# Kernel tuning notes

Measured on AMD Instinct MI355X. Metric: run time of the kernel, lower is better.

Reference implementation:

```python
import jax, jax.numpy as jnp
import numpy as np

NEG_SLOPE = 0.1


def _conv3d(x, w, b):
    # standard 3x3x3 conv, stride 1, pad 1, NCDHW layout
    y = jax.lax.conv_general_dilated(
        x, w, window_strides=(1, 1, 1), padding=[(1, 1), (1, 1), (1, 1)],
        dimension_numbers=('NCDHW', 'OIDHW', 'NCDHW'))
    return y + b[None, :, None, None, None]


def _deform_conv3d_hw(x, w_off, b_off, w, b):
    """DeformConvPack_d with dimension='HW': 3x3x3 conv whose H/W sampling
    positions are shifted by learned per-location offsets (bilinear sample in
    H,W; integer taps in D). Zero padding outside the volume."""
    B, C, D, H, W = x.shape
    # offset conv: 2 offsets (dh, dw) per kernel tap, 27 taps -> 54 channels
    off = _conv3d(x, w_off, b_off).reshape(B, 27, 2, D, H, W)
    x_flat = x.reshape(B, C, D * H * W)
    d_grid = jnp.arange(D)[:, None, None]          # [D,1,1]
    h_grid = jnp.arange(H)[None, :, None]          # [1,H,1]
    w_grid = jnp.arange(W)[None, None, :]          # [1,1,W]
    out = jnp.zeros((B, w.shape[0], D, H, W), x.dtype)
    k = 0
    for kd in (-1, 0, 1):
        pd = d_grid + kd                            # integer depth tap
        valid_d = (pd >= 0) & (pd < D)
        pdc = jnp.clip(pd, 0, D - 1)
        for kh in (-1, 0, 1):
            for kw in (-1, 0, 1):
                ph = h_grid + kh + off[:, k, 0]     # [B,D,H,W] float
                pw = w_grid + kw + off[:, k, 1]
                h0 = jnp.floor(ph)
                w0 = jnp.floor(pw)
                th = ph - h0                        # bilinear fracs
                tw = pw - w0
                h0i = h0.astype(jnp.int32)
                w0i = w0.astype(jnp.int32)
                samp = jnp.zeros((B, C, D, H, W), x.dtype)
                for dh, wgt_h in ((0, 1.0 - th), (1, th)):
                    hh = h0i + dh
                    vh = (hh >= 0) & (hh < H)
                    hhc = jnp.clip(hh, 0, H - 1)
                    for dw, wgt_w in ((0, 1.0 - tw), (1, tw)):
                        ww = w0i + dw
                        v = valid_d & vh & (ww >= 0) & (ww < W)
                        wwc = jnp.clip(ww, 0, W - 1)
                        idx = (pdc * H + hhc) * W + wwc          # [B,D,H,W]
                        g = jnp.take_along_axis(
                            x_flat, idx.reshape(B, 1, D * H * W), axis=2
                        ).reshape(B, C, D, H, W)
                        wgt = jnp.where(v, wgt_h * wgt_w, 0.0)
                        samp = samp + g * wgt[:, None]
                # accumulate this tap's contribution through the conv weight
                out = out + jnp.einsum('bcdhw,oc->bodhw', samp,
                                       w[:, :, kd + 1, kh + 1, kw + 1])
                k += 1
    return out + b[None, :, None, None, None]


def setup_inputs() -> dict:
    key = jax.random.key(0)
    ks = jax.random.split(key, 9)
    B, nf, D, H, W = 4, 48, 12, 56, 56
    fan = 1.0 / np.sqrt(nf * 27)
    x = jax.random.normal(ks[0], (B, nf, D, H, W), jnp.float32)
    # offset convs: small weights so sampled offsets stay O(1) pixel
    w_off0 = jax.random.normal(ks[1], (54, nf, 3, 3, 3), jnp.float32) * 0.01
    b_off0 = jax.random.normal(ks[2], (54,), jnp.float32) * 0.01
    w0 = jax.random.normal(ks[3], (nf, nf, 3, 3, 3), jnp.float32) * fan
    b0 = jax.random.normal(ks[4], (nf,), jnp.float32) * 0.01
    w_off1 = jax.random.normal(ks[5], (54, nf, 3, 3, 3), jnp.float32) * 0.01
    b_off1 = jax.random.normal(ks[6], (54,), jnp.float32) * 0.01
    w1 = jax.random.normal(ks[7], (nf, nf, 3, 3, 3), jnp.float32) * fan
    b1 = jax.random.normal(ks[8], (nf,), jnp.float32) * 0.01
    return {"x": x, "w_off0": w_off0, "b_off0": b_off0, "w0": w0, "b0": b0,
            "w_off1": w_off1, "b_off1": b_off1, "w1": w1, "b1": b1}


def reference(x, w_off0, b_off0, w0, b0, w_off1, b_off1, w1, b1):
    h = _deform_conv3d_hw(x, w_off0, b_off0, w0, b0)
    h = jnp.where(h >= 0, h, NEG_SLOPE * h)  # LeakyReLU(0.1)
    y = _deform_conv3d_hw(h, w_off1, b_off1, w1, b1)
    return y + x
```

## Files before the change

### kernel.cpp

```cpp
#include <hip/hip_runtime.h>
#include <hip/hip_bf16.h>

constexpr int B_ = 4, C_ = 48, D_ = 12, H_ = 56, W_ = 56;
constexpr int DHW_ = D_ * H_ * W_;
constexpr int NLOC_ = B_ * DHW_;
constexpr int OFFC_ = 54;
constexpr int NXCD_ = 8;

typedef short bf16x8 __attribute__((ext_vector_type(8)));
typedef float f32x4  __attribute__((ext_vector_type(4)));
typedef unsigned int u32x4 __attribute__((ext_vector_type(4)));
typedef unsigned int u32x2 __attribute__((ext_vector_type(2)));

__device__ __forceinline__ int xcd_swizzle(int bid, int nwg) {
    int xcd = bid % NXCD_, lid = bid / NXCD_;
    int q = nwg / NXCD_, r = nwg % NXCD_;
    return (xcd < r ? xcd * (q + 1) : r * (q + 1) + (xcd - r) * q) + lid;
}

__device__ __forceinline__ unsigned int f2bf_u(float f) {
    __hip_bfloat16 h = __float2bfloat16(f);
    return (unsigned int)__builtin_bit_cast(unsigned short, h);
}
__device__ __forceinline__ float bflo(unsigned int pv) {
    return __builtin_bit_cast(float, pv << 16);
}
__device__ __forceinline__ float bfhi(unsigned int pv) {
    return __builtin_bit_cast(float, pv & 0xffff0000u);
}

__device__ __forceinline__ u32x4 interp4(u32x4 c00, u32x4 c01, u32x4 c10, u32x4 c11,
                                         f32x4 cw) {
    u32x4 pv;
#pragma unroll
    for (int u = 0; u < 4; ++u) {
        float lo = cw[0] * bflo(c00[u]);
        lo = fmaf(cw[1], bflo(c01[u]), lo);
        lo = fmaf(cw[2], bflo(c10[u]), lo);
        lo = fmaf(cw[3], bflo(c11[u]), lo);
        float hi = cw[0] * bfhi(c00[u]);
        hi = fmaf(cw[1], bfhi(c01[u]), hi);
        hi = fmaf(cw[2], bfhi(c10[u]), hi);
        hi = fmaf(cw[3], bfhi(c11[u]), hi);
        pv[u] = f2bf_u(lo) | (f2bf_u(hi) << 16);
    }
    return pv;
}

__global__ void __launch_bounds__(256) repack_frag_kernel(
    const float* __restrict__ w, unsigned short* __restrict__ wf, int OC, int MT) {
    int t = blockIdx.x * 256 + threadIdx.x;
    int total = 27 * MT * 1024;
    if (t >= total) return;
    int i    = t & 7;
    int lane = (t >> 3) & 63;
    int ks   = (t >> 9) & 1;
    int mt   = (t >> 10) % MT;
    int k    = t / (MT << 10);
    int oc = mt * 16 + (lane & 15);
    int c  = ks * 32 + 8 * (lane >> 4) + i;
    float v = (oc < OC && c < 48) ? w[((size_t)oc * 48 + c) * 27 + k] : 0.0f;
    wf[t] = (unsigned short)f2bf_u(v);
}

__global__ void __launch_bounds__(256) to_cl_kernel(const float* __restrict__ x,
                                                    unsigned short* __restrict__ xcl) {
    int loc = blockIdx.x * 256 + threadIdx.x;
    int b = loc / DHW_, s = loc - b * DHW_;
    const float* xp = x + (size_t)b * (C_ * DHW_) + s;
#pragma unroll
    for (int q = 0; q < 6; ++q) {
        float v[8];
#pragma unroll
        for (int u = 0; u < 8; ++u) v[u] = xp[(size_t)(q * 8 + u) * DHW_];
        u32x4 o;
#pragma unroll
        for (int u = 0; u < 4; ++u)
            o[u] = f2bf_u(v[2 * u]) | (f2bf_u(v[2 * u + 1]) << 16);
        *(u32x4*)(xcl + ((size_t)q * NLOC_ + loc) * 8) = o;
    }
}

__global__ void __launch_bounds__(128) offconv_mfma(
    const unsigned short* __restrict__ xcl,
    const unsigned short* __restrict__ wf,
    const float* __restrict__ bo,
    float* __restrict__ off) {
    __shared__ unsigned short S[2][64][64];
    int tid = threadIdx.x, wid = tid >> 6, lane = tid & 63;
    int base = xcd_swizzle(blockIdx.x, gridDim.x) * 64;
    int loc = base + lane;
    int b = loc / DHW_;
    int sp = loc - b * DHW_;
    int w = sp % W_; int t1 = sp / W_;
    int h = t1 % H_; int d = t1 / H_;
    int g = lane >> 4, li = lane & 15, l7 = lane & 7;

    u32x4 z = {0, 0, 0, 0};
    *(u32x4*)&S[wid][lane][(6 ^ l7) * 8] = z;
    *(u32x4*)&S[wid][lane][(7 ^ l7) * 8] = z;

    f32x4 acc[4][4];
#pragma unroll
    for (int mt = 0; mt < 4; ++mt)
#pragma unroll
        for (int nt = 0; nt < 4; ++nt) acc[mt][nt] = (f32x4){0.f, 0.f, 0.f, 0.f};

    const u32x4* plane[6];
#pragma unroll
    for (int q = 0; q < 6; ++q)
        plane[q] = (const u32x4*)(xcl + ((size_t)q * NLOC_ + (size_t)b * DHW_) * 8);

#pragma unroll 1
    for (int i = 0; i < 14; ++i) {
        int k = wid + 2 * i;
        if (k >= 27) break;
        int kd = k / 9 - 1, kh = (k / 3) % 3 - 1, kw = k % 3 - 1;
        int pd = d + kd, ph = h + kh, pw = w + kw;
        bool valid = (pd >= 0) & (pd < D_) & (ph >= 0) & (ph < H_) & (pw >= 0) & (pw < W_);
        int pdc = min(max(pd, 0), D_ - 1);
        int phc = min(max(ph, 0), H_ - 1);
        int pwc = min(max(pw, 0), W_ - 1);
        int pix = (pdc * H_ + phc) * W_ + pwc;
        u32x4 pv[6];
#pragma unroll
        for (int cc = 0; cc < 6; ++cc) pv[cc] = plane[cc][pix];
#pragma unroll
        for (int cc = 0; cc < 6; ++cc) {
            if (!valid) pv[cc] = z;
            *(u32x4*)&S[wid][lane][(cc ^ l7) * 8] = pv[cc];
        }
        const unsigned short* wk = wf + (size_t)k * 4096 + lane * 8;
        bf16x8 a[4][2];
#pragma unroll
        for (int mt = 0; mt < 4; ++mt)
#pragma unroll
            for (int ks = 0; ks < 2; ++ks)
                a[mt][ks] = *(const bf16x8*)&wk[(mt * 2 + ks) * 512];
#pragma unroll
        for (int nt = 0; nt < 4; ++nt) {
            const unsigned short* sr = &S[wid][nt * 16 + li][0];
            bf16x8 b0 = *(const bf16x8*)&sr[((0 + g) ^ l7) * 8];
            bf16x8 b1 = *(const bf16x8*)&sr[((4 + g) ^ l7) * 8];
#pragma unroll
            for (int mt = 0; mt < 4; ++mt) {
                acc[mt][nt] = __builtin_amdgcn_mfma_f32_16x16x32_bf16(a[mt][0], b0, acc[mt][nt], 0, 0, 0);
                acc[mt][nt] = __builtin_amdgcn_mfma_f32_16x16x32_bf16(a[mt][1], b1, acc[mt][nt], 0, 0, 0);
            }
        }
    }

    float* XCH = (float*)&S[0][0][0];
    __syncthreads();
    if (wid == 1) {
#pragma unroll
        for (int mt = 0; mt < 2; ++mt)
#pragma unroll
            for (int nt = 0; nt < 4; ++nt)
                *(f32x4*)(XCH + (mt * 4 + nt) * 256 + lane * 4) = acc[mt][nt];
    }
    __syncthreads();
    if (wid == 0) {
#pragma unroll
        for (int mt = 0; mt < 2; ++mt)
#pragma unroll
            for (int nt = 0; nt < 4; ++nt)
                acc[mt][nt] += *(f32x4*)(XCH + (mt * 4 + nt) * 256 + lane * 4);
    }
    __syncthreads();
    if (wid == 1) {
#pragma unroll
        for (int mt = 2; mt < 4; ++mt)
#pragma unroll
            for (int nt = 0; nt < 4; ++nt)
                *(f32x4*)(XCH + ((mt - 2) * 4 + nt) * 256 + lane * 4) = acc[mt][nt];
    }
    __syncthreads();
    if (wid == 1) return;
#pragma unroll
    for (int mt = 2; mt < 4; ++mt)
#pragma unroll
        for (int nt = 0; nt < 4; ++nt)
            acc[mt][nt] += *(f32x4*)(XCH + ((mt - 2) * 4 + nt) * 256 + lane * 4);

    int s0 = base - b * DHW_;
#pragma unroll
    for (int mt = 0; mt < 4; ++mt) {
#pragma unroll
        for (int r = 0; r < 4; ++r) {
            int oc = mt * 16 + 4 * g + r;
            if (oc < OFFC_) {
                float bb = bo[oc];
#pragma unroll
                for (int nt = 0; nt < 4; ++nt) {
                    size_t addr = ((size_t)b * OFFC_ + oc) * DHW_ + (s0 + nt * 16 + li);
                    off[addr] = acc[mt][nt][r] + bb;
                }
            }
        }
    }
}

template <int LEAKY, int RESID, int CLOUT>
__global__ void __launch_bounds__(128) deform_mfma(
    const unsigned short* __restrict__ scl,
    const float* __restrict__ off,
    const unsigned short* __restrict__ wf,
    const float* __restrict__ bias,
    const float* __restrict__ resid,
    float* __restrict__ dstf,
    unsigned short* __restrict__ dstcl) {
    __shared__ unsigned short S[2][64][64];
    int tid = threadIdx.x, wid = tid >> 6, lane = tid & 63;
    int base = xcd_swizzle(blockIdx.x, gridDim.x) * 64;
    int loc = base + lane;
    int b = loc / DHW_;
    int sp = loc - b * DHW_;
    int w = sp % W_; int t1 = sp / W_;
    int h = t1 % H_; int d = t1 / H_;
    int g = lane >> 4, li = lane & 15, l7 = lane & 7;

    u32x4 z = {0, 0, 0, 0};
    *(u32x4*)&S[wid][lane][(6 ^ l7) * 8] = z;
    *(u32x4*)&S[wid][lane][(7 ^ l7) * 8] = z;

    f32x4 acc[3][4];
#pragma unroll
    for (int mt = 0; mt < 3; ++mt)
#pragma unroll
        for (int nt = 0; nt < 4; ++nt) acc[mt][nt] = (f32x4){0.f, 0.f, 0.f, 0.f};

    const u32x4* plane[6];
#pragma unroll
    for (int q = 0; q < 6; ++q)
        plane[q] = (const u32x4*)(scl + ((size_t)q * NLOC_ + (size_t)b * DHW_) * 8);
    const float* ob = off + (size_t)b * (OFFC_ * DHW_) + sp;

#pragma unroll 1
    for (int i = 0; i < 14; ++i) {
        int k = wid + 2 * i;
        if (k >= 27) break;
        int kd = k / 9 - 1, kh = (k / 3) % 3 - 1, kw = k % 3 - 1;
        int pd = d + kd;
        bool vd = (pd >= 0) & (pd < D_);
        int pdc = min(max(pd, 0), D_ - 1);

        float odh = ob[(size_t)(2 * k + 0) * DHW_];
        float odw = ob[(size_t)(2 * k + 1) * DHW_];
        float phf = (float)(h + kh) + odh;
        float pwf = (float)(w + kw) + odw;
        float h0f = floorf(phf), w0f = floorf(pwf);
        float th = phf - h0f, tw = pwf - w0f;
        int h0 = (int)h0f, w0 = (int)w0f;

        int pix[4];
        f32x4 cw;
#pragma unroll
        for (int dh = 0; dh < 2; ++dh) {
            int hh = h0 + dh;
            bool vh = vd & (hh >= 0) & (hh < H_);
            int hhc = min(max(hh, 0), H_ - 1);
            float wh = dh ? th : 1.0f - th;
#pragma unroll
            for (int dw = 0; dw < 2; ++dw) {
                int ww = w0 + dw;
                bool v = vh & (ww >= 0) & (ww < W_);
                int wwc = min(max(ww, 0), W_ - 1);
                float wwt = dw ? tw : 1.0f - tw;
                pix[dh * 2 + dw] = (pdc * H_ + hhc) * W_ + wwc;
                cw[dh * 2 + dw] = v ? wh * wwt : 0.0f;
            }
        }

#pragma unroll
        for (int half = 0; half < 2; ++half) {
            u32x4 st[3][4];
#pragma unroll
            for (int cc = 0; cc < 3; ++cc)
#pragma unroll
                for (int j = 0; j < 4; ++j)
                    st[cc][j] = plane[half * 3 + cc][pix[j]];
#pragma unroll
            for (int cc = 0; cc < 3; ++cc) {
                u32x4 pv = interp4(st[cc][0], st[cc][1], st[cc][2], st[cc][3], cw);
                *(u32x4*)&S[wid][lane][((half * 3 + cc) ^ l7) * 8] = pv;
            }
        }

        const unsigned short* wk = wf + (size_t)k * 3072 + lane * 8;
        bf16x8 a[3][2];
#pragma unroll
        for (int mt = 0; mt < 3; ++mt)
#pragma unroll
            for (int ks = 0; ks < 2; ++ks)
                a[mt][ks] = *(const bf16x8*)&wk[(mt * 2 + ks) * 512];
#pragma unroll
        for (int nt = 0; nt < 4; ++nt) {
            const unsigned short* sr = &S[wid][nt * 16 + li][0];
            bf16x8 b0 = *(const bf16x8*)&sr[((0 + g) ^ l7) * 8];
            bf16x8 b1 = *(const bf16x8*)&sr[((4 + g) ^ l7) * 8];
#pragma unroll
            for (int mt = 0; mt < 3; ++mt) {
                acc[mt][nt] = __builtin_amdgcn_mfma_f32_16x16x32_bf16(a[mt][0], b0, acc[mt][nt], 0, 0, 0);
                acc[mt][nt] = __builtin_amdgcn_mfma_f32_16x16x32_bf16(a[mt][1], b1, acc[mt][nt], 0, 0, 0);
            }
        }
    }

    float* XCH = (float*)&S[1][0][0];
    __syncthreads();
    if (wid == 1) {
#pragma unroll
        for (int mt = 0; mt < 2; ++mt)
#pragma unroll
            for (int nt = 0; nt < 4; ++nt)
                *(f32x4*)(XCH + (mt * 4 + nt) * 256 + lane * 4) = acc[mt][nt];
    }
    __syncthreads();
    if (wid == 0) {
#pragma unroll
        for (int mt = 0; mt < 2; ++mt)
#pragma unroll
            for (int nt = 0; nt < 4; ++nt)
                acc[mt][nt] += *(f32x4*)(XCH + (mt * 4 + nt) * 256 + lane * 4);
    }
    __syncthreads();
    if (wid == 1) {
#pragma unroll
        for (int nt = 0; nt < 4; ++nt)
            *(f32x4*)(XCH + nt * 256 + lane * 4) = acc[2][nt];
    }
    __syncthreads();
    if (wid == 1) return;
#pragma unroll
    for (int nt = 0; nt < 4; ++nt)
        acc[2][nt] += *(f32x4*)(XCH + nt * 256 + lane * 4);

    if (CLOUT) {
        unsigned short* Sb = &S[0][0][0];
#pragma unroll
        for (int mt = 0; mt < 3; ++mt) {
#pragma unroll
            for (int nt = 0; nt < 4; ++nt) {
                float v[4];
#pragma unroll
                for (int r = 0; r < 4; ++r) {
                    int oc = mt * 16 + 4 * g + r;
                    float t = acc[mt][nt][r] + bias[oc];
                    if (LEAKY) t = (t >= 0.f) ? t : 0.1f * t;
                    v[r] = t;
                }
                int row = nt * 16 + li;
                int colb = (mt * 32 + 8 * g) ^ ((li & 7) << 4);
                u32x2 pp = {f2bf_u(v[0]) | (f2bf_u(v[1]) << 16),
                            f2bf_u(v[2]) | (f2bf_u(v[3]) << 16)};
                *(u32x2*)((char*)(Sb + (size_t)row * 64) + colb) = pp;
            }
        }
        unsigned short* myrow = Sb + (size_t)lane * 64;
#pragma unroll
        for (int s = 0; s < 6; ++s) {
            u32x4 c = *(u32x4*)((char*)myrow + ((s * 16) ^ ((lane & 7) << 4)));
            *(u32x4*)(dstcl + ((size_t)s * NLOC_ + loc) * 8) = c;
        }
    } else {
        int s0 = base - b * DHW_;
#pragma unroll
        for (int mt = 0; mt < 3; ++mt) {
#pragma unroll
            for (int r = 0; r < 4; ++r) {
                int oc = mt * 16 + 4 * g + r;
                float bb = bias[oc];
#pragma unroll
                for (int nt = 0; nt < 4; ++nt) {
                    size_t addr = ((size_t)b * C_ + oc) * DHW_ + (s0 + nt * 16 + li);
                    float v = acc[mt][nt][r] + bb;
                    if (LEAKY) v = (v >= 0.0f) ? v : 0.1f * v;
                    if (RESID) v += resid[addr];
                    dstf[addr] = v;
                }
            }
        }
    }
}

extern "C" void kernel_launch(void* const* d_in, const int* in_sizes, int n_in,
                              void* d_out, int out_size, void* d_ws, size_t ws_size,
                              hipStream_t stream) {
    const float* x      = (const float*)d_in[0];
    const float* w_off0 = (const float*)d_in[1];
    const float* b_off0 = (const float*)d_in[2];
    const float* w0     = (const float*)d_in[3];
    const float* b0     = (const float*)d_in[4];
    const float* w_off1 = (const float*)d_in[5];
    const float* b_off1 = (const float*)d_in[6];
    const float* w1     = (const float*)d_in[7];
    const float* b1     = (const float*)d_in[8];
    float* out = (float*)d_out;

    float* off_buf = (float*)d_ws;
    unsigned short* xcl = (unsigned short*)(off_buf + (size_t)OFFC_ * NLOC_);
    unsigned short* hcl = xcl + (size_t)NLOC_ * 48;
    unsigned short* wf_off  = hcl + (size_t)NLOC_ * 48;
    unsigned short* wf_conv = wf_off + 27 * 4 * 1024;

    dim3 blk128(128), blk256(256);
    int nblk = NLOC_ / 64;

    to_cl_kernel<<<NLOC_ / 256, blk256, 0, stream>>>(x, xcl);

    repack_frag_kernel<<<(27 * 4 * 1024 + 255) / 256, blk256, 0, stream>>>(w_off0, wf_off, OFFC_, 4);
    repack_frag_kernel<<<(27 * 3 * 1024 + 255) / 256, blk256, 0, stream>>>(w0, wf_conv, C_, 3);
    offconv_mfma<<<nblk, blk128, 0, stream>>>(xcl, wf_off, b_off0, off_buf);
    deform_mfma<1, 0, 1><<<nblk, blk128, 0, stream>>>(xcl, off_buf, wf_conv, b0, nullptr, nullptr, hcl);

    repack_frag_kernel<<<(27 * 4 * 1024 + 255) / 256, blk256, 0, stream>>>(w_off1, wf_off, OFFC_, 4);
    repack_frag_kernel<<<(27 * 3 * 1024 + 255) / 256, blk256, 0, stream>>>(w1, wf_conv, C_, 3);
    offconv_mfma<<<nblk, blk128, 0, stream>>>(hcl, wf_off, b_off1, off_buf);
    deform_mfma<0, 1, 0><<<nblk, blk128, 0, stream>>>(hcl, off_buf, wf_conv, b1, x, out, nullptr);
}
```

Before: 296.8 us.

## Fuse offset conv into deformable conv kernel via shared-memory offset tile

Merges the offset-convolution kernel and the deformable-convolution kernel into one per-layer kernel. Offsets for each 64-location tile are computed with MFMA, biased, and stored in a shared-memory tile, so the deform stage reads them from LDS instead of a global offset buffer. This removes the global write and read of the 54-channel fp32 offset tensor and one launch per layer. It also skips kernel taps that are invalid for the whole wavefront. The cost is extra LDS use (about 15 KB more per block), which may lower occupancy, plus more registers and syncs in a single kernel.

```diff
diff --git a/kernel.cpp b/kernel.cpp
--- a/kernel.cpp
+++ b/kernel.cpp
@@ -9,6 +9,7 @@
 
 typedef short bf16x8 __attribute__((ext_vector_type(8)));
 typedef float f32x4  __attribute__((ext_vector_type(4)));
+typedef float f32x2  __attribute__((ext_vector_type(2)));
 typedef unsigned int u32x4 __attribute__((ext_vector_type(4)));
 typedef unsigned int u32x2 __attribute__((ext_vector_type(2)));
 
@@ -81,12 +82,18 @@
     }
 }
 
-__global__ void __launch_bounds__(128) offconv_mfma(
-    const unsigned short* __restrict__ xcl,
-    const unsigned short* __restrict__ wf,
+template <int LEAKY, int RESID, int CLOUT>
+__global__ void __launch_bounds__(128) fused_layer(
+    const unsigned short* __restrict__ scl,
+    const unsigned short* __restrict__ wfo,
     const float* __restrict__ bo,
-    float* __restrict__ off) {
+    const unsigned short* __restrict__ wfc,
+    const float* __restrict__ bias,
+    const float* __restrict__ resid,
+    float* __restrict__ dstf,
+    unsigned short* __restrict__ dstcl) {
     __shared__ unsigned short S[2][64][64];
+    __shared__ __align__(16) float OFT[64][58];
     int tid = threadIdx.x, wid = tid >> 6, lane = tid & 63;
     int base = xcd_swizzle(blockIdx.x, gridDim.x) * 64;
     int loc = base + lane;
@@ -100,127 +107,108 @@
     *(u32x4*)&S[wid][lane][(6 ^ l7) * 8] = z;
     *(u32x4*)&S[wid][lane][(7 ^ l7) * 8] = z;
 
-    f32x4 acc[4][4];
-#pragma unroll
-    for (int mt = 0; mt < 4; ++mt)
-#pragma unroll
-        for (int nt = 0; nt < 4; ++nt) acc[mt][nt] = (f32x4){0.f, 0.f, 0.f, 0.f};
-
     const u32x4* plane[6];
 #pragma unroll
     for (int q = 0; q < 6; ++q)
-        plane[q] = (const u32x4*)(xcl + ((size_t)q * NLOC_ + (size_t)b * DHW_) * 8);
+        plane[q] = (const u32x4*)(scl + ((size_t)q * NLOC_ + (size_t)b * DHW_) * 8);
+
+    {
+        f32x4 acc[4][4];
+#pragma unroll
+        for (int mt = 0; mt < 4; ++mt)
+#pragma unroll
+            for (int nt = 0; nt < 4; ++nt) acc[mt][nt] = (f32x4){0.f, 0.f, 0.f, 0.f};
 
 #pragma unroll 1
-    for (int i = 0; i < 14; ++i) {
-        int k = wid + 2 * i;
-        if (k >= 27) break;
-        int kd = k / 9 - 1, kh = (k / 3) % 3 - 1, kw = k % 3 - 1;
-        int pd = d + kd, ph = h + kh, pw = w + kw;
-        bool valid = (pd >= 0) & (pd < D_) & (ph >= 0) & (ph < H_) & (pw >= 0) & (pw < W_);
-        int pdc = min(max(pd, 0), D_ - 1);
-        int phc = min(max(ph, 0), H_ - 1);
-        int pwc = min(max(pw, 0), W_ - 1);
-        int pix = (pdc * H_ + phc) * W_ + pwc;
-        u32x4 pv[6];
-#pragma unroll
-        for (int cc = 0; cc < 6; ++cc) pv[cc] = plane[cc][pix];
-#pragma unroll
-        for (int cc = 0; cc < 6; ++cc) {
-            if (!valid) pv[cc] = z;
-            *(u32x4*)&S[wid][lane][(cc ^ l7) * 8] = pv[cc];
-        }
-        const unsigned short* wk = wf + (size_t)k * 4096 + lane * 8;
-        bf16x8 a[4][2];
-#pragma unroll
-        for (int mt = 0; mt < 4; ++mt)
-#pragma unroll
-            for (int ks = 0; ks < 2; ++ks)
-                a[mt][ks] = *(const bf16x8*)&wk[(mt * 2 + ks) * 512];
-#pragma unroll
-        for (int nt = 0; nt < 4; ++nt) {
-            const unsigned short* sr = &S[wid][nt * 16 + li][0];
-            bf16x8 b0 = *(const bf16x8*)&sr[((0 + g) ^ l7) * 8];
-            bf16x8 b1 = *(const bf16x8*)&sr[((4 + g) ^ l7) * 8];
-#pragma unroll
-            for (int mt = 0; mt < 4; ++mt) {
-                acc[mt][nt] = __builtin_amdgcn_mfma_f32_16x16x32_bf16(a[mt][0], b0, acc[mt][nt], 0, 0, 0);
-                acc[mt][nt] = __builtin_amdgcn_mfma_f32_16x16x32_bf16(a[mt][1], b1, acc[mt][nt], 0, 0, 0);
-            }
-        }
-    }
-
-    float* XCH = (float*)&S[0][0][0];
-    __syncthreads();
-    if (wid == 1) {
-#pragma unroll
-        for (int mt = 0; mt < 2; ++mt)
-#pragma unroll
-            for (int nt = 0; nt < 4; ++nt)
-                *(f32x4*)(XCH + (mt * 4 + nt) * 256 + lane * 4) = acc[mt][nt];
-    }
-    __syncthreads();
-    if (wid == 0) {
-#pragma unroll
-        for (int mt = 0; mt < 2; ++mt)
-#pragma unroll
-            for (int nt = 0; nt < 4; ++nt)
-                acc[mt][nt] += *(f32x4*)(XCH + (mt * 4 + nt) * 256 + lane * 4);
-    }
-    __syncthreads();
-    if (wid == 1) {
-#pragma unroll
-        for (int mt = 2; mt < 4; ++mt)
-#pragma unroll
-            for (int nt = 0; nt < 4; ++nt)
-                *(f32x4*)(XCH + ((mt - 2) * 4 + nt) * 256 + lane * 4) = acc[mt][nt];
-    }
-    __syncthreads();
-    if (wid == 1) return;
-#pragma unroll
-    for (int mt = 2; mt < 4; ++mt)
-#pragma unroll
-        for (int nt = 0; nt < 4; ++nt)
-            acc[mt][nt] += *(f32x4*)(XCH + ((mt - 2) * 4 + nt) * 256 + lane * 4);
-
-    int s0 = base - b * DHW_;
-#pragma unroll
-    for (int mt = 0; mt < 4; ++mt) {
-#pragma unroll
-        for (int r = 0; r < 4; ++r) {
-            int oc = mt * 16 + 4 * g + r;
-            if (oc < OFFC_) {
-                float bb = bo[oc];
-#pragma unroll
-                for (int nt = 0; nt < 4; ++nt) {
-                    size_t addr = ((size_t)b * OFFC_ + oc) * DHW_ + (s0 + nt * 16 + li);
-                    off[addr] = acc[mt][nt][r] + bb;
+        for (int i = 0; i < 14; ++i) {
+            int k = wid + 2 * i;
+            if (k >= 27) break;
+            int kd = k / 9 - 1, kh = (k / 3) % 3 - 1, kw = k % 3 - 1;
+            int pd = d + kd, ph = h + kh, pw = w + kw;
+            bool valid = (pd >= 0) & (pd < D_) & (ph >= 0) & (ph < H_) &
+                         (pw >= 0) & (pw < W_);
+            if (!__any((int)valid)) continue;
+            int pdc = min(max(pd, 0), D_ - 1);
+            int phc = min(max(ph, 0), H_ - 1);
+            int pwc = min(max(pw, 0), W_ - 1);
+            int pix = (pdc * H_ + phc) * W_ + pwc;
+            u32x4 pv[6];
+#pragma unroll
+            for (int cc = 0; cc < 6; ++cc) pv[cc] = plane[cc][pix];
+#pragma unroll
+            for (int cc = 0; cc < 6; ++cc) {
+                if (!valid) pv[cc] = z;
+                *(u32x4*)&S[wid][lane][(cc ^ l7) * 8] = pv[cc];
+            }
+            const unsigned short* wk = wfo + (size_t)k * 4096 + lane * 8;
+            bf16x8 a[4][2];
+#pragma unroll
+            for (int mt = 0; mt < 4; ++mt)
+#pragma unroll
+                for (int ks = 0; ks < 2; ++ks)
+                    a[mt][ks] = *(const bf16x8*)&wk[(mt * 2 + ks) * 512];
+#pragma unroll
+            for (int nt = 0; nt < 4; ++nt) {
+                const unsigned short* sr = &S[wid][nt * 16 + li][0];
+                bf16x8 b0 = *(const bf16x8*)&sr[((0 + g) ^ l7) * 8];
+                bf16x8 b1 = *(const bf16x8*)&sr[((4 + g) ^ l7) * 8];
+#pragma unroll
+                for (int mt = 0; mt < 4; ++mt) {
+                    acc[mt][nt] = __builtin_amdgcn_mfma_f32_16x16x32_bf16(a[mt][0], b0, acc[mt][nt], 0, 0, 0);
+                    acc[mt][nt] = __builtin_amdgcn_mfma_f32_16x16x32_bf16(a[mt][1], b1, acc[mt][nt], 0, 0, 0);
                 }
             }
         }
-    }
-}
-
-template <int LEAKY, int RESID, int CLOUT>
-__global__ void __launch_bounds__(128) deform_mfma(
-    const unsigned short* __restrict__ scl,
-    const float* __restrict__ off,
-    const unsigned short* __restrict__ wf,
-    const float* __restrict__ bias,
-    const float* __restrict__ resid,
-    float* __restrict__ dstf,
-    unsigned short* __restrict__ dstcl) {
-    __shared__ unsigned short S[2][64][64];
-    int tid = threadIdx.x, wid = tid >> 6, lane = tid & 63;
-    int base = xcd_swizzle(blockIdx.x, gridDim.x) * 64;
-    int loc = base + lane;
-    int b = loc / DHW_;
-    int sp = loc - b * DHW_;
-    int w = sp % W_; int t1 = sp / W_;
-    int h = t1 % H_; int d = t1 / H_;
-    int g = lane >> 4, li = lane & 15, l7 = lane & 7;
-
-    u32x4 z = {0, 0, 0, 0};
+
+        float* XCH = (float*)&S[0][0][0];
+        __syncthreads();
+        if (wid == 1) {
+#pragma unroll
+            for (int mt = 0; mt < 2; ++mt)
+#pragma unroll
+                for (int nt = 0; nt < 4; ++nt)
+                    *(f32x4*)(XCH + (mt * 4 + nt) * 256 + lane * 4) = acc[mt][nt];
+        }
+        __syncthreads();
+        if (wid == 0) {
+#pragma unroll
+            for (int mt = 0; mt < 2; ++mt)
+#pragma unroll
+                for (int nt = 0; nt < 4; ++nt)
+                    acc[mt][nt] += *(f32x4*)(XCH + (mt * 4 + nt) * 256 + lane * 4);
+        }
+        __syncthreads();
+        if (wid == 1) {
+#pragma unroll
+            for (int mt = 2; mt < 4; ++mt)
+#pragma unroll
+                for (int nt = 0; nt < 4; ++nt)
+                    *(f32x4*)(XCH + ((mt - 2) * 4 + nt) * 256 + lane * 4) = acc[mt][nt];
+        }
+        __syncthreads();
+        if (wid == 0) {
+#pragma unroll
+            for (int mt = 2; mt < 4; ++mt)
+#pragma unroll
+                for (int nt = 0; nt < 4; ++nt)
+                    acc[mt][nt] += *(f32x4*)(XCH + ((mt - 2) * 4 + nt) * 256 + lane * 4);
+#pragma unroll
+            for (int mt = 0; mt < 4; ++mt)
+#pragma unroll
+                for (int nt = 0; nt < 4; ++nt)
+#pragma unroll
+                    for (int rp = 0; rp < 2; ++rp) {
+                        int oc = mt * 16 + 4 * g + 2 * rp;
+                        if (oc < OFFC_) {
+                            f32x2 v = {acc[mt][nt][2 * rp] + bo[oc],
+                                       acc[mt][nt][2 * rp + 1] + bo[oc + 1]};
+                            *(f32x2*)&OFT[nt * 16 + li][oc] = v;
+                        }
+                    }
+        }
+        __syncthreads();
+    }
+
     *(u32x4*)&S[wid][lane][(6 ^ l7) * 8] = z;
     *(u32x4*)&S[wid][lane][(7 ^ l7) * 8] = z;
 
@@ -229,12 +217,6 @@
     for (int mt = 0; mt < 3; ++mt)
 #pragma unroll
         for (int nt = 0; nt < 4; ++nt) acc[mt][nt] = (f32x4){0.f, 0.f, 0.f, 0.f};
-
-    const u32x4* plane[6];
-#pragma unroll
-    for (int q = 0; q < 6; ++q)
-        plane[q] = (const u32x4*)(scl + ((size_t)q * NLOC_ + (size_t)b * DHW_) * 8);
-    const float* ob = off + (size_t)b * (OFFC_ * DHW_) + sp;
 
 #pragma unroll 1
     for (int i = 0; i < 14; ++i) {
@@ -243,12 +225,12 @@
         int kd = k / 9 - 1, kh = (k / 3) % 3 - 1, kw = k % 3 - 1;
         int pd = d + kd;
         bool vd = (pd >= 0) & (pd < D_);
+        if (!__any((int)vd)) continue;
         int pdc = min(max(pd, 0), D_ - 1);
 
-        float odh = ob[(size_t)(2 * k + 0) * DHW_];
-        float odw = ob[(size_t)(2 * k + 1) * DHW_];
-        float phf = (float)(h + kh) + odh;
-        float pwf = (float)(w + kw) + odw;
+        f32x2 od = *(const f32x2*)&OFT[lane][2 * k];
+        float phf = (float)(h + kh) + od.x;
+        float pwf = (float)(w + kw) + od.y;
         float h0f = floorf(phf), w0f = floorf(pwf);
         float th = phf - h0f, tw = pwf - w0f;
         int h0 = (int)h0f, w0 = (int)w0f;
@@ -287,7 +269,7 @@
             }
         }
 
-        const unsigned short* wk = wf + (size_t)k * 3072 + lane * 8;
+        const unsigned short* wk = wfc + (size_t)k * 3072 + lane * 8;
         bf16x8 a[3][2];
 #pragma unroll
         for (int mt = 0; mt < 3; ++mt)
@@ -398,8 +380,7 @@
     const float* b1     = (const float*)d_in[8];
     float* out = (float*)d_out;
 
-    float* off_buf = (float*)d_ws;
-    unsigned short* xcl = (unsigned short*)(off_buf + (size_t)OFFC_ * NLOC_);
+    unsigned short* xcl = (unsigned short*)d_ws;
     unsigned short* hcl = xcl + (size_t)NLOC_ * 48;
     unsigned short* wf_off  = hcl + (size_t)NLOC_ * 48;
     unsigned short* wf_conv = wf_off + 27 * 4 * 1024;
@@ -411,11 +392,11 @@
 
     repack_frag_kernel<<<(27 * 4 * 1024 + 255) / 256, blk256, 0, stream>>>(w_off0, wf_off, OFFC_, 4);
     repack_frag_kernel<<<(27 * 3 * 1024 + 255) / 256, blk256, 0, stream>>>(w0, wf_conv, C_, 3);
-    offconv_mfma<<<nblk, blk128, 0, stream>>>(xcl, wf_off, b_off0, off_buf);
-    deform_mfma<1, 0, 1><<<nblk, blk128, 0, stream>>>(xcl, off_buf, wf_conv, b0, nullptr, nullptr, hcl);
+    fused_layer<1, 0, 1><<<nblk, blk128, 0, stream>>>(xcl, wf_off, b_off0, wf_conv, b0,
+                                                      nullptr, nullptr, hcl);
 
     repack_frag_kernel<<<(27 * 4 * 1024 + 255) / 256, blk256, 0, stream>>>(w_off1, wf_off, OFFC_, 4);
     repack_frag_kernel<<<(27 * 3 * 1024 + 255) / 256, blk256, 0, stream>>>(w1, wf_conv, C_, 3);
-    offconv_mfma<<<nblk, blk128, 0, stream>>>(hcl, wf_off, b_off1, off_buf);
-    deform_mfma<0, 1, 0><<<nblk, blk128, 0, stream>>>(hcl, off_buf, wf_conv, b1, x, out, nullptr);
-}
+    fused_layer<0, 1, 0><<<nblk, blk128, 0, stream>>>(hcl, wf_off, b_off1, wf_conv, b1,
+                                                      x, out, nullptr);
+}
```

After: 293.1 us. About the same (-1.2%).
